# Kernel tuning notes

Measured on AMD Instinct MI355X. Metric: run time of the kernel, lower is better.

The kernel has to match this reference:

```python
import jax, jax.numpy as jnp
import numpy as np

EPS = 1e-5
N_EXPERTS = 8
TOP_K = 2
FEATURE_DIM = 3920   # 20 * 14 * 14 for 3x64x64 input
HIDDEN = 128
GATE_HIDDEN = 64     # hidden_dim // 2
OUT_DIM = 1000


def conv2d(x, w, b, pad):
    # x: [N,C,H,W], w: [O,I,kh,kw]
    y = jax.lax.conv_general_dilated(
        x, w, window_strides=(1, 1), padding=[(pad, pad), (pad, pad)],
        dimension_numbers=("NCHW", "OIHW", "NCHW"))
    return y + b[None, :, None, None]


def maxpool2(x):
    return jax.lax.reduce_window(x, -jnp.inf, jax.lax.max,
                                 (1, 1, 2, 2), (1, 1, 2, 2), "VALID")


def batchnorm(x, gamma, beta):
    # training-mode batch statistics (deterministic), matching nn.BatchNorm2d math
    mean = x.mean(axis=(0, 2, 3), keepdims=True)
    var = x.var(axis=(0, 2, 3), keepdims=True)
    return (x - mean) * jax.lax.rsqrt(var + EPS) * gamma[None, :, None, None] + beta[None, :, None, None]


def setup_inputs() -> dict:
    key = jax.random.key(0)
    ks = jax.random.split(key, 20)
    s = 0.02
    inp = {
        "x": jax.random.normal(ks[0], (4096, 3, 64, 64), dtype=jnp.float32),
        "conv1_w": jax.random.normal(ks[1], (10, 3, 5, 5), dtype=jnp.float32) * s,
        "conv1_b": jnp.zeros((10,), jnp.float32),
        "bn_g": jnp.ones((10,), jnp.float32),
        "bn_b": jnp.zeros((10,), jnp.float32),
        "conv2_w": jax.random.normal(ks[2], (20, 10, 5, 5), dtype=jnp.float32) * s,
        "conv2_b": jnp.zeros((20,), jnp.float32),
        "gate_w1": jax.random.normal(ks[3], (GATE_HIDDEN, FEATURE_DIM), dtype=jnp.float32) * s,
        "gate_b1": jnp.zeros((GATE_HIDDEN,), jnp.float32),
        "gate_w2": jax.random.normal(ks[4], (N_EXPERTS, GATE_HIDDEN), dtype=jnp.float32) * s,
        "gate_b2": jnp.zeros((N_EXPERTS,), jnp.float32),
        # stacked expert weights: E experts, fc1 F->H, fc2 H->H/2, fc3 H/2->O
        "ew1": jax.random.normal(ks[5], (N_EXPERTS, HIDDEN, FEATURE_DIM), dtype=jnp.float32) * s,
        "eb1": jnp.zeros((N_EXPERTS, HIDDEN), jnp.float32),
        "ew2": jax.random.normal(ks[6], (N_EXPERTS, HIDDEN // 2, HIDDEN), dtype=jnp.float32) * s,
        "eb2": jnp.zeros((N_EXPERTS, HIDDEN // 2), jnp.float32),
        "ew3": jax.random.normal(ks[7], (N_EXPERTS, OUT_DIM, HIDDEN // 2), dtype=jnp.float32) * s,
        "eb3": jnp.zeros((N_EXPERTS, OUT_DIM), jnp.float32),
    }
    return inp


def reference(x, conv1_w, conv1_b, bn_g, bn_b, conv2_w, conv2_b,
              gate_w1, gate_b1, gate_w2, gate_b2,
              ew1, eb1, ew2, eb2, ew3, eb3):
    B = x.shape[0]
    # feature extractor (input cast to complex64 in torch has zero imag part,
    # so the complex path is numerically identical to real arithmetic)
    f = jax.nn.relu(batchnorm(conv2d(x, conv1_w, conv1_b, 1), bn_g, bn_b))
    f = maxpool2(f)
    f = jax.nn.relu(conv2d(f, conv2_w, conv2_b, 1))
    f = maxpool2(f)
    feat = f.reshape(B, -1)  # [B, 3920]

    # gate operates on |features| (complex abs -> |real|)
    g = jax.nn.relu(jnp.abs(feat) @ gate_w1.T + gate_b1)
    logits = g @ gate_w2.T + gate_b2               # [B, E]
    vals, idx = jax.lax.top_k(logits, TOP_K)
    topk_g = jax.nn.softmax(vals, axis=-1)
    gates = jnp.zeros_like(logits).at[jnp.arange(B)[:, None], idx].set(topk_g)

    # dense all-expert compute (matches torch loop: every expert runs full batch,
    # combined with gate weights that are zero for unselected experts)
    h = jax.nn.relu(jnp.einsum("bf,ehf->beh", feat, ew1) + eb1)   # [B,E,128]
    h = jax.nn.relu(jnp.einsum("beh,egh->beg", h, ew2) + eb2)     # [B,E,64]
    eo = jnp.einsum("beg,eog->beo", h, ew3) + eb3                  # [B,E,O]
    out = jnp.einsum("beo,be->bo", eo, gates)                      # [B,O]
    return jax.nn.log_softmax(jnp.abs(out), axis=1)
```

## Files before the change

kernel.cpp:

```cpp
#include <hip/hip_runtime.h>
#include <hip/hip_bf16.h>


#define TPB 256

typedef __attribute__((ext_vector_type(8))) short bf16x8;
typedef __attribute__((ext_vector_type(4))) float f32x4;
typedef __attribute__((ext_vector_type(16))) float f32x16;

__device__ __forceinline__ float bf2f(unsigned short u) {
  return __uint_as_float(((unsigned)u) << 16);
}
__device__ __forceinline__ ushort f2b(float f) {
  __hip_bfloat16 h = __float2bfloat16(f);
  return *(ushort*)&h;
}

__global__ __launch_bounds__(TPB) void k_conv1(
    const float* __restrict__ x, const float* __restrict__ w1c,
    const float* __restrict__ b1c, __hip_bfloat16* __restrict__ pool1,
    float* __restrict__ stats)
{
  __shared__ ushort img[3 * 66 * 68];
  __shared__ ushort slc[9 * 64 * 18];
  __shared__ float sred[20];
  const int tid = threadIdx.x;
  const int lane = tid & 63;
  const int w = tid >> 6;
  const int n = blockIdx.x;
  const int oc = lane & 15;
  const int q = lane >> 4;

  {
    uint* p = (uint*)img;
    for (int i = tid; i < 6732; i += TPB) p[i] = 0;
    uint* z = (uint*)slc;
    for (int i = tid; i < 5184; i += TPB) z[i] = 0;
    if (tid < 20) sred[tid] = 0.f;
  }
  __syncthreads();

  {
    const float* xp = x + (size_t)n * 12288;
#pragma unroll
    for (int it = 0; it < 12; it++) {
      const int e = 4 * (tid + 256 * it);
      const float4 v = *(const float4*)(xp + e);
      const int ic = e >> 12, rem = e & 4095, row = rem >> 6, col = rem & 63;
      ushort* d = &img[ic * 4488 + (row + 1) * 68 + (col + 1)];
      d[0] = f2b(v.x); d[1] = f2b(v.y); d[2] = f2b(v.z); d[3] = f2b(v.w);
    }
  }

  bf16x8 bfrag[3];
#pragma unroll
  for (int ch = 0; ch < 3; ch++) {
    union { ushort s[8]; bf16x8 v; } bu;
#pragma unroll
    for (int j = 0; j < 8; j++) {
      const int k15 = (q & 1) * 8 + j;
      const int kh = 2 * ch + (q >> 1);
      float wv = 0.f;
      if (oc < 10 && k15 < 15 && kh < 5) {
        const int ic = (k15 >= 10) ? 2 : ((k15 >= 5) ? 1 : 0);
        const int kw = k15 - ic * 5;
        wv = w1c[oc * 75 + ic * 25 + kh * 5 + kw];
      }
      bu.s[j] = f2b(wv);
    }
    bfrag[ch] = bu.v;
  }
  const float bias = (oc < 10) ? b1c[oc] : 0.f;

  int bsrc[4], bdst[4], bcnt = 0;
#pragma unroll
  for (int j = 0; j < 4; j++) {
    const int k15 = w + 4 * j;
    if (k15 < 15) {
      const int ic = (k15 >= 10) ? 2 : ((k15 >= 5) ? 1 : 0);
      const int kw = k15 - ic * 5;
      bsrc[bcnt] = ic * 4488 + kw + lane;
      bdst[bcnt] = lane * 18 + k15;
      bcnt++;
    }
  }

  __syncthreads();

  for (int t = 0; t < 4; t++) {
    ushort* sb = &slc[(t & 7) * 1152];
    const int tof = t * 68;
    for (int j = 0; j < bcnt; j++) sb[bdst[j]] = img[bsrc[j] + tof];
  }

  const int c0 = w * 16;
  const int fofs = (c0 + oc) * 18 + (q & 1) * 8;
  const bool qlo = (q < 2);
  float vm[4];
#pragma unroll
  for (int i = 0; i < 4; i++)
    vm[i] = ((c0 + q * 4 + i) < 62) ? 1.f : 0.f;

  float ts = 0.f, tss = 0.f;
  float pp0 = 0.f, pp1 = 0.f;

  for (int r = 0; r < 62; r++) {
    {
      const int t = r + 4;
      ushort* sb = &slc[(t & 7) * 1152];
      const int tof = t * 68;
      for (int j = 0; j < bcnt; j++) sb[bdst[j]] = img[bsrc[j] + tof];
    }
    __syncthreads();

    f32x4 acc = {0.f, 0.f, 0.f, 0.f};
#pragma unroll
    for (int ch = 0; ch < 3; ch++) {
      const int sa = (r + 2 * ch) & 7;
      const int sb2 = (ch == 2) ? 8 : ((r + 2 * ch + 1) & 7);
      const ushort* base = &slc[(qlo ? sa : sb2) * 1152 + fofs];
      union { uint u[4]; bf16x8 v; } au;
      au.u[0] = *(const uint*)(base + 0);
      au.u[1] = *(const uint*)(base + 2);
      au.u[2] = *(const uint*)(base + 4);
      au.u[3] = *(const uint*)(base + 6);
      acc = __builtin_amdgcn_mfma_f32_16x16x32_bf16(au.v, bfrag[ch], acc, 0, 0, 0);
    }

    const float y0 = acc[0] + bias, y1 = acc[1] + bias;
    const float y2 = acc[2] + bias, y3 = acc[3] + bias;
    float t0 = y0 * vm[0]; ts += t0; tss = fmaf(t0, y0, tss);
    float t1 = y1 * vm[1]; ts += t1; tss = fmaf(t1, y1, tss);
    float t2 = y2 * vm[2]; ts += t2; tss = fmaf(t2, y2, tss);
    float t3 = y3 * vm[3]; ts += t3; tss = fmaf(t3, y3, tss);
    const float p0v = fmaxf(y0, y1), p1v = fmaxf(y2, y3);
    if ((r & 1) == 0) {
      pp0 = p0v; pp1 = p1v;
    } else if (oc < 10) {
      const int ph = r >> 1;
      const int pwb = (c0 >> 1) + q * 2;
      __hip_bfloat16* dst = pool1 + (size_t)n * 9610 + (size_t)(ph * 31) * 10 + oc;
      const float q0 = fmaxf(pp0, p0v), q1 = fmaxf(pp1, p1v);
      dst[pwb * 10] = __float2bfloat16(q0);
      if (pwb + 1 < 31) dst[(pwb + 1) * 10] = __float2bfloat16(q1);
    }
  }

  if (oc < 10) {
    atomicAdd(&sred[oc], ts);
    atomicAdd(&sred[10 + oc], tss);
  }
  __syncthreads();
  if (tid < 20) atomicAdd(&stats[tid], sred[tid]);
}

__global__ void k_bnfin(const float* __restrict__ bng,
                        const float* __restrict__ bnb,
                        float* __restrict__ stats)
{
  const int c = threadIdx.x;
  if (c < 10) {
    const float Ninv = 1.f / (4096.f * 3844.f);
    const float mean = stats[c] * Ninv;
    const float var = stats[10 + c] * Ninv - mean * mean;
    const float sc = bng[c] * rsqrtf(var + 1e-5f);
    stats[20 + c] = sc;
    stats[30 + c] = bnb[c] - mean * sc;
  }
}

__global__ __launch_bounds__(TPB, 2) void k_conv2(
    const __hip_bfloat16* __restrict__ pool1, const float* __restrict__ stats,
    const float* __restrict__ w2c, const float* __restrict__ b2c,
    __hip_bfloat16* __restrict__ featb)
{
  __shared__ ushort R[4][4][344];
  __shared__ float ssc[10], ssh[10];
  const int tid = threadIdx.x;
  const int w = tid >> 6, lane = tid & 63;
  const int n = blockIdx.x * 4 + w;
  const int pos = lane & 31, q = lane >> 5;
  ushort (*Rw)[344] = R[w];

  if (tid < 10) { ssc[tid] = stats[20 + tid]; ssh[tid] = stats[30 + tid]; }
  for (int i = lane; i < 136; i += 64) {
    const int s = i / 34, uu = i - 34 * s;
    Rw[s][(uu < 10) ? uu : (310 + uu)] = 0;
  }
  if (lane < 60) {
    uint* z = (uint*)((ushort*)featb + (size_t)n * 4160 + 3920);
    z[lane] = 0; z[lane + 60] = 0;
  }
  __syncthreads();

  bf16x8 wf[20];
#pragma unroll
  for (int kk = 0; kk < 20; kk++) {
    union { ushort u[8]; bf16x8 v; } bu;
    const int s = kk >> 2;
#pragma unroll
    for (int i = 0; i < 8; i++) {
      const int j = (kk & 3) * 16 + q * 8 + i;
      float wv = 0.f;
      if ((pos < 20) && (j < 50))
        wv = w2c[pos * 250 + (j % 10) * 25 + s * 5 + (j / 10)];
      bu.u[i] = f2b(wv);
    }
    wf[kk] = bu.v;
  }
  const float bias = (pos < 20) ? b2c[pos] : 0.f;

  const ushort* pp = (const ushort*)pool1 + (size_t)n * 9610;
  const int ic0 = (2 * lane) % 10;
  const int pos_e = (pos < 28) ? pos : pos - 16;
  const int pe10q8 = pos_e * 10 + q * 8;

  uint gv0, gv1, gv2;
#define GLOAD(t)                                                        \
  {                                                                     \
    const ushort* s_ = pp + ((t) - 1) * 310;                            \
    gv0 = *(const uint*)(s_ + 2 * lane);                                \
    gv1 = *(const uint*)(s_ + 2 * (lane + 64));                         \
    gv2 = (lane < 27) ? *(const uint*)(s_ + 2 * (lane + 128)) : 0u;     \
  }
#define GS1(c_, gv_)                                                    \
  {                                                                     \
    const int u2_ = lane + 64 * c_;                                     \
    if (c_ < 2 || lane < 27) {                                          \
      const int ia_ = (ic0 + 8 * c_) % 10;                              \
      const int ib_ = (ia_ == 9) ? 0 : ia_ + 1;                         \
      float a0_ = bf2f((ushort)(gv_ & 0xffffu));                        \
      float a1_ = bf2f((ushort)(gv_ >> 16));                            \
      a0_ = fmaxf(fmaf(a0_, ssc[ia_], ssh[ia_]), 0.f);                  \
      a1_ = fmaxf(fmaf(a1_, ssc[ib_], ssh[ib_]), 0.f);                  \
      *(uint*)(dst_ + 2 * u2_) = (uint)f2b(a0_) | ((uint)f2b(a1_) << 16);\
    }                                                                   \
  }
#define GSTORE(t)                                                       \
  {                                                                     \
    ushort* dst_ = &Rw[(t) & 3][10];                                    \
    GS1(0, gv0) GS1(1, gv1) GS1(2, gv2)                                 \
  }
#define FLOAD(t, ss)                                                    \
  {                                                                     \
    const ushort* bp_ = &Rw[(t) & 3][pe10q8];                           \
    _Pragma("unroll")                                                   \
    for (int sub_ = 0; sub_ < 4; sub_++) {                              \
      union { uint u[4]; bf16x8 v; } au_;                               \
      au_.u[0] = *(const uint*)(bp_ + sub_ * 16 + 0);                   \
      au_.u[1] = *(const uint*)(bp_ + sub_ * 16 + 2);                   \
      au_.u[2] = *(const uint*)(bp_ + sub_ * 16 + 4);                   \
      au_.u[3] = *(const uint*)(bp_ + sub_ * 16 + 6);                   \
      sets[ss][sub_] = au_.v;                                           \
    }                                                                   \
  }

  bf16x8 sets[5][4];
  const bf16x8 zfrag = (short)0;
#pragma unroll
  for (int s = 0; s < 4; s++) sets[0][s] = zfrag;

  GLOAD(1) GSTORE(1)
  GLOAD(2) GSTORE(2)
  GLOAD(3) GSTORE(3)
  GLOAD(4) GSTORE(4)
  GLOAD(5)
  __asm__ __volatile__("s_waitcnt lgkmcnt(0)" ::: "memory");
  FLOAD(1, 1) FLOAD(2, 2) FLOAD(3, 3)

  float php[8];
  for (int rb = 0; rb < 30; rb += 5) {
#pragma unroll
    for (int rr = 0; rr < 5; rr++) {
      const int r = rb + rr;
      __asm__ __volatile__("s_waitcnt lgkmcnt(0)" ::: "memory");
      if (r <= 27) FLOAD(r + 4, (rr + 4) % 5)
      if (r <= 26) GSTORE(r + 5)
      if (r <= 25) GLOAD(r + 6)
      if (r < 28) {
        f32x16 accA, accB;
#pragma unroll
        for (int z = 0; z < 16; z++) { accA[z] = 0.f; accB[z] = 0.f; }
#pragma unroll
        for (int kh = 0; kh < 5; kh++) {
          const int si = (rr + kh) % 5;
#pragma unroll
          for (int sub = 0; sub < 4; sub++) {
            if (kh & 1)
              accB = __builtin_amdgcn_mfma_f32_32x32x16_bf16(
                  sets[si][sub], wf[kh * 4 + sub], accB, 0, 0, 0);
            else
              accA = __builtin_amdgcn_mfma_f32_32x32x16_bf16(
                  sets[si][sub], wf[kh * 4 + sub], accA, 0, 0, 0);
          }
        }
        float hp[8];
#pragma unroll
        for (int p = 0; p < 8; p++)
          hp[p] = fmaxf(accA[2 * p] + accB[2 * p],
                        accA[2 * p + 1] + accB[2 * p + 1]);
        if ((r & 1) == 0) {
#pragma unroll
          for (int p = 0; p < 8; p++) php[p] = hp[p];
        } else if (pos < 20) {
          const int ph = r >> 1;
          ushort* dst = (ushort*)featb + (size_t)n * 4160 + pos * 196 + ph * 14;
#pragma unroll
          for (int j = 0; j < 4; j++) {
            const int pw = 4 * j + 2 * q;
            if (pw + 1 < 14) {
              const float v0 =
                  fmaxf(fmaxf(php[2 * j], hp[2 * j]) + bias, 0.f);
              const float v1 =
                  fmaxf(fmaxf(php[2 * j + 1], hp[2 * j + 1]) + bias, 0.f);
              *(uint*)(dst + pw) = (uint)f2b(v0) | ((uint)f2b(v1) << 16);
            }
          }
        }
      }
    }
  }
#undef GLOAD
#undef GS1
#undef GSTORE
#undef FLOAD
}

__global__ __launch_bounds__(TPB) void k_castw1(
    const float* __restrict__ ew1, ushort* __restrict__ w1b)
{
  const int o = blockIdx.x;
  const int tid = threadIdx.x;
  const float* srow = ew1 + (size_t)o * 3920;
  ushort* drow = w1b + (size_t)o * 4160;
  for (int i = tid; i < 1040; i += TPB) {
    const int k4 = i * 4;
    ushort4 r;
    if (k4 < 3920) {
      const float4 v = *(const float4*)(srow + k4);
      r.x = f2b(v.x); r.y = f2b(v.y); r.z = f2b(v.z); r.w = f2b(v.w);
    } else {
      r.x = 0; r.y = 0; r.z = 0; r.w = 0;
    }
    *(ushort4*)(drow + k4) = r;
  }
}

__global__ __launch_bounds__(TPB) void k_gate1(
    const ushort* __restrict__ featb, const float* __restrict__ gw1,
    float* __restrict__ graw)
{
  __shared__ float sf[64 * 113];
  __shared__ float sw[64 * 113];
  const int tid = threadIdx.x;
  const int r0 = blockIdx.x * 64;
  const int kz = blockIdx.y;
  const int ty = tid >> 4, tx = tid & 15;
  float acc[4][4] = {{0.f}};
  for (int c = kz; c < 35; c += 4) {
    const int k0 = c * 112;
    for (int i = tid; i < 896; i += TPB) {
      const int row = i / 14, k8 = (i - row * 14) * 8;
      uint4 v = *(const uint4*)(featb + (size_t)(r0 + row) * 4160 + k0 + k8);
      const ushort* pv = (const ushort*)&v;
      float* d = &sf[row * 113 + k8];
#pragma unroll
      for (int t = 0; t < 8; t++) d[t] = bf2f(pv[t]);
    }
    for (int i = tid; i < 1792; i += TPB) {
      const int row = i / 28, c4 = (i - row * 28) * 4;
      float4 u = *(const float4*)(gw1 + (size_t)row * 3920 + k0 + c4);
      float* e = &sw[row * 113 + c4];
      e[0] = u.x; e[1] = u.y; e[2] = u.z; e[3] = u.w;
    }
    __syncthreads();
    for (int k = 0; k < 112; k++) {
      float a_[4], w_[4];
#pragma unroll
      for (int i = 0; i < 4; i++) a_[i] = sf[(ty * 4 + i) * 113 + k];
#pragma unroll
      for (int j = 0; j < 4; j++) w_[j] = sw[(tx * 4 + j) * 113 + k];
#pragma unroll
      for (int i = 0; i < 4; i++)
#pragma unroll
        for (int j = 0; j < 4; j++) acc[i][j] = fmaf(a_[i], w_[j], acc[i][j]);
    }
    __syncthreads();
  }
#pragma unroll
  for (int i = 0; i < 4; i++)
#pragma unroll
    for (int j = 0; j < 4; j++)
      atomicAdd(&graw[(size_t)(r0 + ty * 4 + i) * 64 + tx * 4 + j], acc[i][j]);
}

__global__ __launch_bounds__(TPB) void k_gate2(
    const float* __restrict__ graw, const float* __restrict__ gb1,
    const float* __restrict__ gw2, const float* __restrict__ gb2,
    int* __restrict__ sel0, int* __restrict__ sel1,
    float* __restrict__ wt0, float* __restrict__ wt1, int* __restrict__ counts)
{
  __shared__ float sw2[512], sb1[64], sb2[8];
  const int tid = threadIdx.x;
  for (int i = tid; i < 512; i += TPB) sw2[i] = gw2[i];
  if (tid < 64) sb1[tid] = gb1[tid];
  if (tid < 8) sb2[tid] = gb2[tid];
  __syncthreads();
  const int r = blockIdx.x * TPB + tid;
  float l[8];
#pragma unroll
  for (int c = 0; c < 8; c++) l[c] = sb2[c];
  const float* gr = graw + (size_t)r * 64;
  for (int k = 0; k < 64; k++) {
    const float hv = fmaxf(gr[k] + sb1[k], 0.f);
#pragma unroll
    for (int c = 0; c < 8; c++) l[c] = fmaf(hv, sw2[c * 64 + k], l[c]);
  }
  float v0 = -1e30f, v1 = -1e30f; int i0 = 0, i1 = 0;
#pragma unroll
  for (int c = 0; c < 8; c++) {
    const float lv = l[c];
    if (lv > v0) { v1 = v0; i1 = i0; v0 = lv; i0 = c; }
    else if (lv > v1) { v1 = lv; i1 = c; }
  }
  const float e1 = expf(v1 - v0);
  const float inv = 1.f / (1.f + e1);
  sel0[r] = i0; sel1[r] = i1; wt0[r] = inv; wt1[r] = e1 * inv;
  atomicAdd(&counts[i0], 1);
  atomicAdd(&counts[i1], 1);
}

__global__ void k_prep(int* __restrict__ hdrI, int* __restrict__ entrow)
{
  const int tid = threadIdx.x;
  if (tid == 0) {
    int run = 0;
    for (int e = 0; e < 8; e++) {
      const int c = hdrI[e];
      const int pc = (c + 31) & ~31;
      hdrI[16 + e] = pc;
      hdrI[24 + e] = run;
      run += pc;
    }
    hdrI[32] = run;
  }
  if (tid >= 8 && tid < 16) hdrI[tid] = 0;
  for (int i = tid; i < 8448; i += TPB) entrow[i] = -1;
}

__global__ void k_scatter(const int* __restrict__ sel0, const int* __restrict__ sel1,
                          int* __restrict__ hdrI, int* __restrict__ entrow,
                          int* __restrict__ p0, int* __restrict__ p1)
{
  const int r = blockIdx.x * TPB + threadIdx.x;
  const int e0 = sel0[r];
  int pos = atomicAdd(&hdrI[8 + e0], 1) + hdrI[24 + e0];
  entrow[pos] = r; p0[r] = pos;
  const int e1 = sel1[r];
  pos = atomicAdd(&hdrI[8 + e1], 1) + hdrI[24 + e1];
  entrow[pos] = r; p1[r] = pos;
}

__global__ __launch_bounds__(512) void k_fc1(
    const ushort* __restrict__ featb, const ushort* __restrict__ w1b,
    const float* __restrict__ eb1, __hip_bfloat16* __restrict__ h1b)
{
  __shared__ ushort As[128 * 72];
  __shared__ ushort Bs[128 * 72];
  const int tid = threadIdx.x;
  const int r0 = blockIdx.x * 128;
  const int c0 = blockIdx.y * 128;
  const int w = tid >> 6, lane = tid & 63;
  const int wr = (w >> 1) * 32, wc = (w & 1) * 64;
  const int m = lane & 15, q = lane >> 4;
  f32x4 acc[2][4];
#pragma unroll
  for (int i = 0; i < 2; i++)
#pragma unroll
    for (int j = 0; j < 4; j++) acc[i][j] = 0.f;

  for (int kc = 0; kc < 4096; kc += 64) {
#pragma unroll
    for (int i = 0; i < 2; i++) {
      const int u = tid + 512 * i;
      const int row = u >> 3, k8 = (u & 7) * 8;
      *(uint4*)(&As[row * 72 + k8]) =
          *(const uint4*)(featb + (size_t)(r0 + row) * 4160 + kc + k8);
      *(uint4*)(&Bs[row * 72 + k8]) =
          *(const uint4*)(w1b + (size_t)(c0 + row) * 4160 + kc + k8);
    }
    __syncthreads();
#pragma unroll
    for (int kk = 0; kk < 64; kk += 32) {
      bf16x8 af[2], bf[4];
#pragma unroll
      for (int t = 0; t < 2; t++)
        af[t] = *(const bf16x8*)(&As[(wr + t * 16 + m) * 72 + kk + q * 8]);
#pragma unroll
      for (int t = 0; t < 4; t++)
        bf[t] = *(const bf16x8*)(&Bs[(wc + t * 16 + m) * 72 + kk + q * 8]);
#pragma unroll
      for (int ti = 0; ti < 2; ti++)
#pragma unroll
        for (int tj = 0; tj < 4; tj++)
          acc[ti][tj] = __builtin_amdgcn_mfma_f32_16x16x32_bf16(
              af[ti], bf[tj], acc[ti][tj], 0, 0, 0);
    }
    __syncthreads();
  }
#pragma unroll
  for (int tj = 0; tj < 4; tj++) {
    const int c = c0 + wc + tj * 16 + m;
    const float bb = eb1[c];
#pragma unroll
    for (int ti = 0; ti < 2; ti++) {
      const int rbase = r0 + wr + ti * 16 + q * 4;
#pragma unroll
      for (int i = 0; i < 4; i++) {
        const float v = fmaxf(acc[ti][tj][i] + bb, 0.f);
        h1b[(size_t)(rbase + i) * 1024 + c] = __float2bfloat16(v);
      }
    }
  }
}

__global__ __launch_bounds__(TPB) void k_fc2(
    const __hip_bfloat16* __restrict__ h1b, const float* __restrict__ ew2,
    const float* __restrict__ eb2, float* __restrict__ h2)
{
  __shared__ float h1s[64 * 132];
  __shared__ ushort w2s[128 * 72];
  const int tid = threadIdx.x;
  const int r0 = blockIdx.x * 64;
  const int e = blockIdx.y;
  const ushort* hp = (const ushort*)h1b;
#pragma unroll
  for (int i = 0; i < 4; i++) {
    const int u = tid + 256 * i;
    const int row = u >> 4, k8 = (u & 15) * 8;
    uint4 v = *(const uint4*)(hp + (size_t)(r0 + row) * 1024 + e * 128 + k8);
    const ushort* pv = (const ushort*)&v;
    float* d = &h1s[row * 132 + k8];
#pragma unroll
    for (int t = 0; t < 8; t++) d[t] = bf2f(pv[t]);
  }
#pragma unroll
  for (int i = 0; i < 8; i++) {
    const int u = tid + 256 * i;
    const int nn = u >> 5, k4 = (u & 31) * 4;
    const float4 v = *(const float4*)(ew2 + (size_t)e * 8192 + nn * 128 + k4);
    w2s[(k4 + 0) * 72 + nn] = f2b(v.x);
    w2s[(k4 + 1) * 72 + nn] = f2b(v.y);
    w2s[(k4 + 2) * 72 + nn] = f2b(v.z);
    w2s[(k4 + 3) * 72 + nn] = f2b(v.w);
  }
  __syncthreads();
  const int ty = tid >> 4, tx = tid & 15;
  float acc[4][4] = {{0.f}};
  for (int k4 = 0; k4 < 32; k4++) {
    f32x4 a4[4];
#pragma unroll
    for (int i = 0; i < 4; i++)
      a4[i] = *(const f32x4*)(&h1s[(ty * 4 + i) * 132 + k4 * 4]);
#pragma unroll
    for (int kk = 0; kk < 4; kk++) {
      const ushort4 wu = *(const ushort4*)(&w2s[(k4 * 4 + kk) * 72 + tx * 4]);
      const float w0 = bf2f(wu.x), w1 = bf2f(wu.y);
      const float w2_ = bf2f(wu.z), w3 = bf2f(wu.w);
#pragma unroll
      for (int i = 0; i < 4; i++) {
        acc[i][0] = fmaf(a4[i][kk], w0, acc[i][0]);
        acc[i][1] = fmaf(a4[i][kk], w1, acc[i][1]);
        acc[i][2] = fmaf(a4[i][kk], w2_, acc[i][2]);
        acc[i][3] = fmaf(a4[i][kk], w3, acc[i][3]);
      }
    }
  }
  const f32x4 bb = *(const f32x4*)(eb2 + e * 64 + tx * 4);
#pragma unroll
  for (int i = 0; i < 4; i++) {
    f32x4 r;
#pragma unroll
    for (int j = 0; j < 4; j++) r[j] = fmaxf(acc[i][j] + bb[j], 0.f);
    *(f32x4*)(h2 + (size_t)(r0 + ty * 4 + i) * 512 + e * 64 + tx * 4) = r;
  }
}

__global__ __launch_bounds__(TPB) void k_fc3(
    const float* __restrict__ h2, const float* __restrict__ ew3,
    const float* __restrict__ eb3, const int* __restrict__ hdrI,
    const int* __restrict__ entrow, float* __restrict__ eo)
{
  __shared__ float h2s[32 * 68];
  __shared__ float w3s[64 * 132];
  const int e = blockIdx.y;
  const int pcnt = hdrI[16 + e];
  if ((int)blockIdx.x * 32 >= pcnt) return;
  const int base = hdrI[24 + e] + blockIdx.x * 32;
  const int tid = threadIdx.x;
  for (int i = tid; i < 512; i += TPB) {
    const int row = i >> 4, k4 = (i & 15) * 4;
    const int rr = entrow[base + row];
    f32x4 v = 0.f;
    if (rr >= 0) v = *(const f32x4*)(h2 + (size_t)rr * 512 + e * 64 + k4);
    *(f32x4*)(&h2s[row * 68 + k4]) = v;
  }
  const int ty = tid >> 5, tx = tid & 31;
  const float* w3p = ew3 + (size_t)e * 64000;
  const float* b3p = eb3 + (size_t)e * 1000;
  for (int nc = 0; nc < 8; nc++) {
    const int o0 = nc * 128;
    for (int i = tid; i < 2048; i += TPB) {
      const int oo = i >> 4, k4 = (i & 15) * 4;
      const int o = o0 + oo;
      f32x4 u = 0.f;
      if (o < 1000) u = *(const f32x4*)(w3p + (size_t)o * 64 + k4);
      w3s[(k4 + 0) * 132 + oo] = u[0];
      w3s[(k4 + 1) * 132 + oo] = u[1];
      w3s[(k4 + 2) * 132 + oo] = u[2];
      w3s[(k4 + 3) * 132 + oo] = u[3];
    }
    __syncthreads();
    float acc[4][4] = {{0.f}};
    for (int k4 = 0; k4 < 16; k4++) {
      f32x4 a4[4], w4[4];
#pragma unroll
      for (int i = 0; i < 4; i++)
        a4[i] = *(const f32x4*)(&h2s[(ty * 4 + i) * 68 + k4 * 4]);
#pragma unroll
      for (int kk = 0; kk < 4; kk++)
        w4[kk] = *(const f32x4*)(&w3s[(k4 * 4 + kk) * 132 + tx * 4]);
#pragma unroll
      for (int kk = 0; kk < 4; kk++)
#pragma unroll
        for (int i = 0; i < 4; i++)
#pragma unroll
          for (int j = 0; j < 4; j++)
            acc[i][j] = fmaf(a4[i][kk], w4[kk][j], acc[i][j]);
    }
    const int o = o0 + tx * 4;
    if (o + 3 < 1000) {
      const f32x4 bb = *(const f32x4*)(b3p + o);
#pragma unroll
      for (int i = 0; i < 4; i++) {
        f32x4 r;
#pragma unroll
        for (int j = 0; j < 4; j++) r[j] = acc[i][j] + bb[j];
        *(f32x4*)(eo + (size_t)(base + ty * 4 + i) * 1000 + o) = r;
      }
    }
    __syncthreads();
  }
}

__global__ __launch_bounds__(TPB) void k_out(
    const float* __restrict__ eo, const int* __restrict__ p0,
    const int* __restrict__ p1, const float* __restrict__ wt0,
    const float* __restrict__ wt1, float* __restrict__ out)
{
  __shared__ float sv[1000];
  __shared__ float sr[8];
  const int r = blockIdx.x, tid = threadIdx.x;
  const float w0 = wt0[r], w1 = wt1[r];
  const float* a = eo + (size_t)p0[r] * 1000;
  const float* b = eo + (size_t)p1[r] * 1000;
  float lmax = -3.4e38f;
  for (int o = tid; o < 1000; o += TPB) {
    const float v = fabsf(w0 * a[o] + w1 * b[o]);
    sv[o] = v;
    lmax = fmaxf(lmax, v);
  }
#pragma unroll
  for (int off = 32; off; off >>= 1) lmax = fmaxf(lmax, __shfl_down(lmax, off));
  if ((tid & 63) == 0) sr[tid >> 6] = lmax;
  __syncthreads();
  const float mx = fmaxf(fmaxf(sr[0], sr[1]), fmaxf(sr[2], sr[3]));
  float lsum = 0.f;
  for (int o = tid; o < 1000; o += TPB) lsum += expf(sv[o] - mx);
#pragma unroll
  for (int off = 32; off; off >>= 1) lsum += __shfl_down(lsum, off);
  if ((tid & 63) == 0) sr[4 + (tid >> 6)] = lsum;
  __syncthreads();
  const float lse = logf(sr[4] + sr[5] + sr[6] + sr[7]);
  const float sub = mx + lse;
  for (int o = tid; o < 1000; o += TPB)
    out[(size_t)r * 1000 + o] = sv[o] - sub;
}

extern "C" void kernel_launch(void* const* d_in, const int* in_sizes, int n_in,
                              void* d_out, int out_size, void* d_ws, size_t ws_size,
                              hipStream_t stream)
{
  (void)in_sizes; (void)n_in; (void)out_size; (void)ws_size;
  const float* x   = (const float*)d_in[0];
  const float* c1w = (const float*)d_in[1];
  const float* c1b = (const float*)d_in[2];
  const float* bng = (const float*)d_in[3];
  const float* bnb = (const float*)d_in[4];
  const float* c2w = (const float*)d_in[5];
  const float* c2b = (const float*)d_in[6];
  const float* gw1 = (const float*)d_in[7];
  const float* gb1 = (const float*)d_in[8];
  const float* gw2 = (const float*)d_in[9];
  const float* gb2 = (const float*)d_in[10];
  const float* ew1 = (const float*)d_in[11];
  const float* eb1 = (const float*)d_in[12];
  const float* ew2 = (const float*)d_in[13];
  const float* eb2 = (const float*)d_in[14];
  const float* ew3 = (const float*)d_in[15];
  const float* eb3 = (const float*)d_in[16];

  char* ws = (char*)d_ws;
  float* statsF = (float*)ws;
  int*   hdrI   = (int*)(ws + 256);
  int*   sel0   = (int*)(ws + 1024);
  int*   sel1   = (int*)(ws + 17408);
  float* wt0    = (float*)(ws + 33792);
  float* wt1    = (float*)(ws + 50176);
  int*   p0     = (int*)(ws + 66560);
  int*   p1     = (int*)(ws + 82944);
  int*   entrow = (int*)(ws + 99328);
  float* graw   = (float*)(ws + 133120);
  float* eo     = (float*)(ws + 1181696);
  __hip_bfloat16* h1b = (__hip_bfloat16*)(ws + 34973696);
  float* h2     = (float*)(ws + 43362304);
  __hip_bfloat16* pool1 = (__hip_bfloat16*)(ws + 51750912);
  __hip_bfloat16* featb = (__hip_bfloat16*)(ws + 130476032);
  ushort* w1b   = (ushort*)(ws + 164554752);

  hipMemsetAsync(ws, 0, 512, stream);
  hipMemsetAsync(graw, 0, 4096 * 64 * sizeof(float), stream);

  k_castw1 <<<1024, TPB, 0, stream>>>(ew1, w1b);
  k_conv1  <<<4096, TPB, 0, stream>>>(x, c1w, c1b, pool1, statsF);
  k_bnfin  <<<1, 64, 0, stream>>>(bng, bnb, statsF);
  k_conv2  <<<1024, TPB, 0, stream>>>(pool1, statsF, c2w, c2b, featb);
  k_gate1  <<<dim3(64, 4), TPB, 0, stream>>>((const ushort*)featb, gw1, graw);
  k_gate2  <<<16, TPB, 0, stream>>>(graw, gb1, gw2, gb2, sel0, sel1, wt0, wt1, hdrI);
  k_prep   <<<1, TPB, 0, stream>>>(hdrI, entrow);
  k_scatter<<<16, TPB, 0, stream>>>(sel0, sel1, hdrI, entrow, p0, p1);
  k_fc1    <<<dim3(32, 8), 512, 0, stream>>>((const ushort*)featb, w1b, eb1, h1b);
  k_fc2    <<<dim3(64, 8), TPB, 0, stream>>>(h1b, ew2, eb2, h2);
  k_fc3    <<<dim3(128, 8), TPB, 0, stream>>>(h2, ew3, eb3, hdrI, entrow, eo);
  k_out    <<<4096, TPB, 0, stream>>>(eo, p0, p1, wt0, wt1, (float*)d_out);
}
```

Baseline: 1.077 ms.

## Restructure conv1 to channel-interleaved LDS image with per-row MFMA and register ring

Stores the padded input image in LDS with the three channels interleaved per pixel, so each MFMA A-fragment is a direct contiguous read. This removes the separate im2col slice buffer, its per-row rebuild, and the per-row __syncthreads. The K dimension becomes (kw, ic) per kernel row, giving five MFMAs per output row into two accumulators, and a five-deep register ring of A fragments is reused across rows. It also shrinks LDS use and adds a waves-per-EU hint to raise occupancy, at the cost of padding waste in K (20 of 32 lanes used) and more MFMAs per row.

```diff
diff --git a/kernel.cpp b/kernel.cpp
--- a/kernel.cpp
+++ b/kernel.cpp
@@ -16,26 +16,25 @@
   return *(ushort*)&h;
 }
 
-__global__ __launch_bounds__(TPB) void k_conv1(
+__global__ __launch_bounds__(TPB, 4) void k_conv1(
     const float* __restrict__ x, const float* __restrict__ w1c,
     const float* __restrict__ b1c, __hip_bfloat16* __restrict__ pool1,
     float* __restrict__ stats)
 {
-  __shared__ ushort img[3 * 66 * 68];
-  __shared__ ushort slc[9 * 64 * 18];
+  __shared__ uint4 imgI4[2183];
   __shared__ float sred[20];
+  ushort* imgI = (ushort*)imgI4;
   const int tid = threadIdx.x;
   const int lane = tid & 63;
   const int w = tid >> 6;
   const int n = blockIdx.x;
   const int oc = lane & 15;
   const int q = lane >> 4;
+  const int c0 = w * 16;
 
   {
-    uint* p = (uint*)img;
-    for (int i = tid; i < 6732; i += TPB) p[i] = 0;
-    uint* z = (uint*)slc;
-    for (int i = tid; i < 5184; i += TPB) z[i] = 0;
+    const uint4 z = {0u, 0u, 0u, 0u};
+    for (int i = tid; i < 2183; i += TPB) imgI4[i] = z;
     if (tid < 20) sred[tid] = 0.f;
   }
   __syncthreads();
@@ -43,59 +42,57 @@
   {
     const float* xp = x + (size_t)n * 12288;
 #pragma unroll
-    for (int it = 0; it < 12; it++) {
-      const int e = 4 * (tid + 256 * it);
-      const float4 v = *(const float4*)(xp + e);
-      const int ic = e >> 12, rem = e & 4095, row = rem >> 6, col = rem & 63;
-      ushort* d = &img[ic * 4488 + (row + 1) * 68 + (col + 1)];
-      d[0] = f2b(v.x); d[1] = f2b(v.y); d[2] = f2b(v.z); d[3] = f2b(v.w);
-    }
-  }
-
-  bf16x8 bfrag[3];
-#pragma unroll
-  for (int ch = 0; ch < 3; ch++) {
-    union { ushort s[8]; bf16x8 v; } bu;
-#pragma unroll
-    for (int j = 0; j < 8; j++) {
-      const int k15 = (q & 1) * 8 + j;
-      const int kh = 2 * ch + (q >> 1);
+    for (int it = 0; it < 4; it++) {
+      const int g = tid + 256 * it;
+      const int row = g >> 4, col0 = (g & 15) * 4;
+      const float4 v0 = *(const float4*)(xp + row * 64 + col0);
+      const float4 v1 = *(const float4*)(xp + 4096 + row * 64 + col0);
+      const float4 v2 = *(const float4*)(xp + 8192 + row * 64 + col0);
+      ushort* d = &imgI[((row + 1) * 66 + (col0 + 1)) * 4];
+      uint2 t0, t1, t2, t3;
+      t0.x = (uint)f2b(v0.x) | ((uint)f2b(v1.x) << 16); t0.y = (uint)f2b(v2.x);
+      t1.x = (uint)f2b(v0.y) | ((uint)f2b(v1.y) << 16); t1.y = (uint)f2b(v2.y);
+      t2.x = (uint)f2b(v0.z) | ((uint)f2b(v1.z) << 16); t2.y = (uint)f2b(v2.z);
+      t3.x = (uint)f2b(v0.w) | ((uint)f2b(v1.w) << 16); t3.y = (uint)f2b(v2.w);
+      *(uint2*)(d + 0)  = t0;
+      *(uint2*)(d + 4)  = t1;
+      *(uint2*)(d + 8)  = t2;
+      *(uint2*)(d + 12) = t3;
+    }
+  }
+
+  bf16x8 wf[5];
+#pragma unroll
+  for (int kh = 0; kh < 5; kh++) {
+    union { ushort u[8]; bf16x8 v; } bu;
+#pragma unroll
+    for (int i = 0; i < 8; i++) {
+      const int j = q * 8 + i;
       float wv = 0.f;
-      if (oc < 10 && k15 < 15 && kh < 5) {
-        const int ic = (k15 >= 10) ? 2 : ((k15 >= 5) ? 1 : 0);
-        const int kw = k15 - ic * 5;
-        wv = w1c[oc * 75 + ic * 25 + kh * 5 + kw];
-      }
-      bu.s[j] = f2b(wv);
-    }
-    bfrag[ch] = bu.v;
+      if (oc < 10 && j < 20 && (j & 3) < 3)
+        wv = w1c[oc * 75 + (j & 3) * 25 + kh * 5 + (j >> 2)];
+      bu.u[i] = f2b(wv);
+    }
+    wf[kh] = bu.v;
   }
   const float bias = (oc < 10) ? b1c[oc] : 0.f;
 
-  int bsrc[4], bdst[4], bcnt = 0;
-#pragma unroll
-  for (int j = 0; j < 4; j++) {
-    const int k15 = w + 4 * j;
-    if (k15 < 15) {
-      const int ic = (k15 >= 10) ? 2 : ((k15 >= 5) ? 1 : 0);
-      const int kw = k15 - ic * 5;
-      bsrc[bcnt] = ic * 4488 + kw + lane;
-      bdst[bcnt] = lane * 18 + k15;
-      bcnt++;
-    }
-  }
-
   __syncthreads();
 
-  for (int t = 0; t < 4; t++) {
-    ushort* sb = &slc[(t & 7) * 1152];
-    const int tof = t * 68;
-    for (int j = 0; j < bcnt; j++) sb[bdst[j]] = img[bsrc[j] + tof];
-  }
-
-  const int c0 = w * 16;
-  const int fofs = (c0 + oc) * 18 + (q & 1) * 8;
-  const bool qlo = (q < 2);
+  const int pos_A = c0 + oc;
+  const ushort* abase = &imgI[pos_A * 4 + q * 8];
+
+#define ALOAD(t, s)                                                     \
+  {                                                                     \
+    const ushort* p_ = abase + (t) * 264;                               \
+    union { uint u[4]; bf16x8 v; } au_;                                 \
+    const uint2 lo_ = *(const uint2*)(p_);                              \
+    const uint2 hi_ = *(const uint2*)(p_ + 4);                          \
+    au_.u[0] = lo_.x; au_.u[1] = lo_.y;                                 \
+    au_.u[2] = hi_.x; au_.u[3] = hi_.y;                                 \
+    sets[s] = au_.v;                                                    \
+  }
+
   float vm[4];
 #pragma unroll
   for (int i = 0; i < 4; i++)
@@ -104,47 +101,52 @@
   float ts = 0.f, tss = 0.f;
   float pp0 = 0.f, pp1 = 0.f;
 
-  for (int r = 0; r < 62; r++) {
-    {
-      const int t = r + 4;
-      ushort* sb = &slc[(t & 7) * 1152];
-      const int tof = t * 68;
-      for (int j = 0; j < bcnt; j++) sb[bdst[j]] = img[bsrc[j] + tof];
-    }
-    __syncthreads();
-
-    f32x4 acc = {0.f, 0.f, 0.f, 0.f};
-#pragma unroll
-    for (int ch = 0; ch < 3; ch++) {
-      const int sa = (r + 2 * ch) & 7;
-      const int sb2 = (ch == 2) ? 8 : ((r + 2 * ch + 1) & 7);
-      const ushort* base = &slc[(qlo ? sa : sb2) * 1152 + fofs];
-      union { uint u[4]; bf16x8 v; } au;
-      au.u[0] = *(const uint*)(base + 0);
-      au.u[1] = *(const uint*)(base + 2);
-      au.u[2] = *(const uint*)(base + 4);
-      au.u[3] = *(const uint*)(base + 6);
-      acc = __builtin_amdgcn_mfma_f32_16x16x32_bf16(au.v, bfrag[ch], acc, 0, 0, 0);
-    }
-
-    const float y0 = acc[0] + bias, y1 = acc[1] + bias;
-    const float y2 = acc[2] + bias, y3 = acc[3] + bias;
-    float t0 = y0 * vm[0]; ts += t0; tss = fmaf(t0, y0, tss);
-    float t1 = y1 * vm[1]; ts += t1; tss = fmaf(t1, y1, tss);
-    float t2 = y2 * vm[2]; ts += t2; tss = fmaf(t2, y2, tss);
-    float t3 = y3 * vm[3]; ts += t3; tss = fmaf(t3, y3, tss);
-    const float p0v = fmaxf(y0, y1), p1v = fmaxf(y2, y3);
-    if ((r & 1) == 0) {
-      pp0 = p0v; pp1 = p1v;
-    } else if (oc < 10) {
-      const int ph = r >> 1;
-      const int pwb = (c0 >> 1) + q * 2;
-      __hip_bfloat16* dst = pool1 + (size_t)n * 9610 + (size_t)(ph * 31) * 10 + oc;
-      const float q0 = fmaxf(pp0, p0v), q1 = fmaxf(pp1, p1v);
-      dst[pwb * 10] = __float2bfloat16(q0);
-      if (pwb + 1 < 31) dst[(pwb + 1) * 10] = __float2bfloat16(q1);
-    }
-  }
+  bf16x8 sets[5];
+  ALOAD(0, 0) ALOAD(1, 1) ALOAD(2, 2) ALOAD(3, 3)
+
+  for (int rb = 0; rb < 62; rb += 5) {
+#pragma unroll
+    for (int rr = 0; rr < 5; rr++) {
+      const int r = rb + rr;
+      if (r < 62) {
+        ALOAD(r + 4, (rr + 4) % 5)
+        f32x4 accA = {0.f, 0.f, 0.f, 0.f};
+        f32x4 accB = {0.f, 0.f, 0.f, 0.f};
+        accA = __builtin_amdgcn_mfma_f32_16x16x32_bf16(
+            sets[(rr + 0) % 5], wf[0], accA, 0, 0, 0);
+        accB = __builtin_amdgcn_mfma_f32_16x16x32_bf16(
+            sets[(rr + 1) % 5], wf[1], accB, 0, 0, 0);
+        accA = __builtin_amdgcn_mfma_f32_16x16x32_bf16(
+            sets[(rr + 2) % 5], wf[2], accA, 0, 0, 0);
+        accB = __builtin_amdgcn_mfma_f32_16x16x32_bf16(
+            sets[(rr + 3) % 5], wf[3], accB, 0, 0, 0);
+        accA = __builtin_amdgcn_mfma_f32_16x16x32_bf16(
+            sets[(rr + 4) % 5], wf[4], accA, 0, 0, 0);
+
+        const float y0 = accA[0] + accB[0] + bias;
+        const float y1 = accA[1] + accB[1] + bias;
+        const float y2 = accA[2] + accB[2] + bias;
+        const float y3 = accA[3] + accB[3] + bias;
+        float t0 = y0 * vm[0]; ts += t0; tss = fmaf(t0, y0, tss);
+        float t1 = y1 * vm[1]; ts += t1; tss = fmaf(t1, y1, tss);
+        float t2 = y2 * vm[2]; ts += t2; tss = fmaf(t2, y2, tss);
+        float t3 = y3 * vm[3]; ts += t3; tss = fmaf(t3, y3, tss);
+        const float p0v = fmaxf(y0, y1), p1v = fmaxf(y2, y3);
+        if ((r & 1) == 0) {
+          pp0 = p0v; pp1 = p1v;
+        } else if (oc < 10) {
+          const int ph = r >> 1;
+          const int pwb = (c0 >> 1) + q * 2;
+          __hip_bfloat16* dst =
+              pool1 + (size_t)n * 9610 + (size_t)(ph * 31) * 10 + oc;
+          const float q0 = fmaxf(pp0, p0v), q1 = fmaxf(pp1, p1v);
+          dst[pwb * 10] = __float2bfloat16(q0);
+          if (pwb + 1 < 31) dst[(pwb + 1) * 10] = __float2bfloat16(q1);
+        }
+      }
+    }
+  }
+#undef ALOAD
 
   if (oc < 10) {
     atomicAdd(&sred[oc], ts);
```

Result: slower. 1.283 ms (+19.1%).
